# Kernel tuning notes

Hardware: AMD Instinct MI355X
Metric: run time of the kernel (lower is better)

The kernel has to match this reference:

```python
import jax, jax.numpy as jnp
from jax import lax
import numpy as np

B, P, ENC, DEC, ATT, E, S, V = 32, 196, 512, 512, 512, 256, 128, 10000

def setup_inputs() -> dict:
    key = jax.random.key(0)
    ks = jax.random.split(key, 20)
    g = lambda k, shape, s=0.02: jax.random.normal(k, shape, dtype=jnp.float32) * s
    return {
        'features': jax.random.normal(ks[0], (B, P, ENC), dtype=jnp.float32),
        'captions': jax.random.randint(ks[1], (B, S), 0, V, dtype=jnp.int64),
        'emb': g(ks[2], (V, E)),
        'W_enc_att': g(ks[3], (ENC, ATT)), 'b_enc_att': jnp.zeros((ATT,), jnp.float32),
        'W_dec_att': g(ks[4], (DEC, ATT)), 'b_dec_att': jnp.zeros((ATT,), jnp.float32),
        'v_att': g(ks[5], (ATT,)), 'b_full_att': jnp.zeros((), jnp.float32),
        'W_init_h': g(ks[6], (ENC, DEC)), 'b_init_h': jnp.zeros((DEC,), jnp.float32),
        'W_init_c': g(ks[7], (ENC, DEC)), 'b_init_c': jnp.zeros((DEC,), jnp.float32),
        'W_ih': g(ks[8], (4 * DEC, E + ENC)), 'W_hh': g(ks[9], (4 * DEC, DEC)),
        'b_ih': jnp.zeros((4 * DEC,), jnp.float32), 'b_hh': jnp.zeros((4 * DEC,), jnp.float32),
        'W_fcn': g(ks[10], (DEC, V)), 'b_fcn': jnp.zeros((V,), jnp.float32),
    }

def reference(features, captions, emb, W_enc_att, b_enc_att, W_dec_att, b_dec_att,
              v_att, b_full_att, W_init_h, b_init_h, W_init_c, b_init_c,
              W_ih, W_hh, b_ih, b_hh, W_fcn, b_fcn):
    # init hidden state from mean encoder features
    mean_f = features.mean(axis=1)                    # [B, ENC]
    h = mean_f @ W_init_h + b_init_h                  # [B, DEC]
    c = mean_f @ W_init_c + b_init_c
    embeds = emb[captions]                            # [B, S, E]
    feat_proj = features @ W_enc_att + b_enc_att      # [B, P, ATT], loop-invariant

    def step(carry, emb_t):
        h, c = carry
        # additive attention: tanh(Uf + Wh) . v -> softmax -> weighted sum
        att = jnp.tanh(feat_proj + (h @ W_dec_att + b_dec_att)[:, None, :])  # [B, P, ATT]
        scores = att @ v_att + b_full_att             # [B, P]
        alpha = jax.nn.softmax(scores, axis=1)
        context = jnp.einsum('bp,bpe->be', alpha, features)  # [B, ENC]
        x = jnp.concatenate([emb_t, context], axis=1)  # [B, E+ENC]
        gates = x @ W_ih.T + b_ih + h @ W_hh.T + b_hh  # [B, 4*DEC]
        i, f, g, o = jnp.split(gates, 4, axis=1)
        c_new = jax.nn.sigmoid(f) * c + jax.nn.sigmoid(i) * jnp.tanh(g)
        h_new = jax.nn.sigmoid(o) * jnp.tanh(c_new)
        out = h_new @ W_fcn + b_fcn                    # dropout = identity (eval)
        return (h_new, c_new), out

    xs = jnp.swapaxes(embeds[:, :S - 1], 0, 1)         # [S-1, B, E]
    _, preds = lax.scan(step, (h, c), xs)              # [S-1, B, V]
    return jnp.swapaxes(preds, 0, 1)                   # [B, S-1, V]
```

## Files before the change

kernel.cpp:

```cpp
#include <hip/hip_runtime.h>
#include <hip/hip_bf16.h>
#include <stdint.h>

#define BB 32
#define PP 196
#define ENC 512
#define DEC 512
#define ATTD 512
#define EE 256
#define SS 128
#define VV 10000
#define TT 127
#define NBLK 512

typedef unsigned short ushort_t;
typedef unsigned int uint_t;
typedef unsigned long long u64_t;
typedef float f32x4 __attribute__((ext_vector_type(4)));
typedef short s16x8 __attribute__((ext_vector_type(8)));

__device__ __forceinline__ float bf2f(ushort_t u) {
    uint_t x = ((uint_t)u) << 16;
    return __uint_as_float(x);
}
__device__ __forceinline__ float bflo(uint_t u) { return __uint_as_float(u << 16); }
__device__ __forceinline__ float bfhi(uint_t u) { return __uint_as_float(u & 0xffff0000u); }
__device__ __forceinline__ ushort_t f2bf(float f) {
    uint_t u = __float_as_uint(f);
    uint_t r = (u + 0x7FFFu + ((u >> 16) & 1u)) >> 16;
    return (ushort_t)r;
}
__device__ __forceinline__ float ftanh(float x) {
    x = fminf(15.f, fmaxf(-15.f, x));
    float e = __expf(2.f * x);
    return (e - 1.f) / (e + 1.f);
}
__device__ __forceinline__ float fsig(float x) {
    return 1.f / (1.f + __expf(-x));
}

__device__ __forceinline__ float aload1(const float* p) {
    return __hip_atomic_load(p, __ATOMIC_RELAXED, __HIP_MEMORY_SCOPE_AGENT);
}
__device__ __forceinline__ void astore1(float* p, float v) {
    __hip_atomic_store(p, v, __ATOMIC_RELAXED, __HIP_MEMORY_SCOPE_AGENT);
}
__device__ __forceinline__ float2 aload2(const float* p) {
    u64_t v = __hip_atomic_load((const u64_t*)p, __ATOMIC_RELAXED, __HIP_MEMORY_SCOPE_AGENT);
    float2 r;
    r.x = __uint_as_float((uint_t)v);
    r.y = __uint_as_float((uint_t)(v >> 32));
    return r;
}


__global__ void k_cvt(const float* __restrict__ s, ushort_t* __restrict__ d, int n) {
    for (int i = blockIdx.x * blockDim.x + threadIdx.x; i < n; i += gridDim.x * blockDim.x)
        d[i] = f2bf(s[i]);
}

__global__ void k_cvtD(const float* __restrict__ Wdec, ushort_t* __restrict__ out) {
    const int n = DEC * ATTD;
    for (int i = blockIdx.x * blockDim.x + threadIdx.x; i < n; i += gridDim.x * blockDim.x) {
        int k = i & (ATTD - 1);
        int j = i >> 9;
        out[i] = f2bf(Wdec[(size_t)k * ATTD + j]);
    }
}

__global__ void k_embed_bf(const int* __restrict__ cap, const float* __restrict__ emb,
                           ushort_t* __restrict__ out) {
    const int n = TT * BB * EE;
    for (int i = blockIdx.x * blockDim.x + threadIdx.x; i < n; i += gridDim.x * blockDim.x) {
        int e = i & (EE - 1);
        int b = (i >> 8) & (BB - 1);
        int t = i >> 13;
        int tok = cap[b * SS + t];
        out[i] = f2bf(emb[(size_t)tok * EE + e]);
    }
}

__global__ void k_cvtT(const float* __restrict__ Wih, ushort_t* __restrict__ out) {
    const int n = EE * 4 * DEC;
    for (int i = blockIdx.x * blockDim.x + threadIdx.x; i < n; i += gridDim.x * blockDim.x) {
        int k = i & (EE - 1);
        int row = i >> 8;
        out[(size_t)k * (4 * DEC) + row] = f2bf(Wih[(size_t)row * (EE + ENC) + k]);
    }
}

__global__ void k_cvtG2(const float* __restrict__ Wih, const float* __restrict__ Whh,
                        ushort_t* __restrict__ out) {
    const int n = 16 * 2 * 64 * 128 * 8;
    for (int i = blockIdx.x * blockDim.x + threadIdx.x; i < n; i += gridDim.x * blockDim.x) {
        int j = i & 7;
        int R = (i >> 3) & 127;
        int kc = (i >> 10) & 63;
        int kh = (i >> 16) & 1;
        int pcg = i >> 17;
        int d = pcg * 32 + (R >> 2);
        int gate = R & 3;
        int row = gate * DEC + d;
        int k = kh * 512 + kc * 8 + j;
        float v = (k < 512) ? Wih[(size_t)row * (EE + ENC) + EE + k]
                            : Whh[(size_t)row * DEC + (k - 512)];
        out[i] = f2bf(v);
    }
}

__global__ void k_bsum(const float* __restrict__ a, const float* __restrict__ b,
                       float* __restrict__ o, int n) {
    int i = blockIdx.x * blockDim.x + threadIdx.x;
    if (i < n) o[i] = a[i] + b[i];
}

__global__ __launch_bounds__(256) void k_init(const float* __restrict__ feat,
                                              const float* __restrict__ Wh, const float* __restrict__ bh,
                                              const float* __restrict__ Wc, const float* __restrict__ bc,
                                              float* __restrict__ h0, float* __restrict__ c0,
                                              int* __restrict__ bar) {
    __shared__ float ms[ENC];
    int b = blockIdx.x, t = threadIdx.x;
    if (b == 0) {
        for (int i = t; i < 4096; i += 256) bar[i] = 0;
    }
    for (int c = t; c < ENC; c += 256) {
        float s = 0.f;
        for (int p = 0; p < PP; ++p) s += feat[((size_t)b * PP + p) * ENC + c];
        ms[c] = s * (1.f / (float)PP);
    }
    __syncthreads();
    int d0 = 2 * t;
    float ah0 = 0.f, ah1 = 0.f, ac0 = 0.f, ac1 = 0.f;
    for (int k = 0; k < ENC; ++k) {
        float mk = ms[k];
        float2 wh = *(const float2*)(Wh + (size_t)k * DEC + d0);
        float2 wc = *(const float2*)(Wc + (size_t)k * DEC + d0);
        ah0 += mk * wh.x; ah1 += mk * wh.y;
        ac0 += mk * wc.x; ac1 += mk * wc.y;
    }
    h0[b * DEC + d0] = ah0 + bh[d0];
    h0[b * DEC + d0 + 1] = ah1 + bh[d0 + 1];
    c0[b * DEC + d0] = ac0 + bc[d0];
    c0[b * DEC + d0 + 1] = ac1 + bc[d0 + 1];
}

template <int MODE>
__global__ __launch_bounds__(256) void k_gemm(const ushort_t* __restrict__ A,
                                              const ushort_t* __restrict__ Bm,
                                              const float* __restrict__ bias,
                                              ushort_t* __restrict__ outb,
                                              float* __restrict__ outf,
                                              int M, int N, int K) {
    __shared__ __align__(16) ushort_t As[128 * 32];
    __shared__ __align__(16) ushort_t Bs[128 * 32];

    const int tid = threadIdx.x;
    const int wid = tid >> 6, lane = tid & 63;
    const int wm = wid >> 1, wn = wid & 1;
    const int lr = lane & 15, lk = (lane >> 4) * 8;
    const int row0 = blockIdx.x * 128, col0 = blockIdx.y * 128;

    f32x4 acc[4][4];
#pragma unroll
    for (int i = 0; i < 4; ++i)
#pragma unroll
        for (int j = 0; j < 4; ++j) acc[i][j] = (f32x4){0.f, 0.f, 0.f, 0.f};

    for (int k0 = 0; k0 < K; k0 += 32) {
        {
            int r = tid >> 1, kk = (tid & 1) * 16;
            int gr = row0 + r;
            uint4 v0 = {0, 0, 0, 0}, v1 = {0, 0, 0, 0};
            if (gr < M) {
                const ushort_t* sp = A + (size_t)gr * K + k0 + kk;
                v0 = *(const uint4*)sp;
                v1 = *(const uint4*)(sp + 8);
            }
            *(uint4*)(As + r * 32 + kk) = v0;
            *(uint4*)(As + r * 32 + kk + 8) = v1;
        }
        {
            int kk = tid >> 3;
            int n = (tid & 7) * 16;
            const ushort_t* sp = Bm + (size_t)(k0 + kk) * N + col0 + n;
            ushort_t tmp[16];
            if (col0 + n + 16 <= N) {
                *(uint4*)tmp = *(const uint4*)sp;
                *(uint4*)(tmp + 8) = *(const uint4*)(sp + 8);
            } else {
#pragma unroll
                for (int j = 0; j < 16; ++j) {
                    int c = col0 + n + j;
                    tmp[j] = (c < N) ? sp[j] : (ushort_t)0;
                }
            }
#pragma unroll
            for (int j = 0; j < 16; ++j) Bs[(n + j) * 32 + kk] = tmp[j];
        }
        __syncthreads();
        s16x8 af[4], bfr[4];
#pragma unroll
        for (int i = 0; i < 4; ++i)
            af[i] = *(const s16x8*)(As + (wm * 64 + i * 16 + lr) * 32 + lk);
#pragma unroll
        for (int j = 0; j < 4; ++j)
            bfr[j] = *(const s16x8*)(Bs + (wn * 64 + j * 16 + lr) * 32 + lk);
#pragma unroll
        for (int i = 0; i < 4; ++i)
#pragma unroll
            for (int j = 0; j < 4; ++j)
                acc[i][j] = __builtin_amdgcn_mfma_f32_16x16x32_bf16(af[i], bfr[j], acc[i][j], 0, 0, 0);
        __syncthreads();
    }

    const int lrow = (lane >> 4) * 4;
#pragma unroll
    for (int i = 0; i < 4; ++i) {
#pragma unroll
        for (int j = 0; j < 4; ++j) {
            int gr0 = row0 + wm * 64 + i * 16 + lrow;
            int gc = col0 + wn * 64 + j * 16 + lr;
#pragma unroll
            for (int r = 0; r < 4; ++r) {
                int gr = gr0 + r;
                if (gr < M && gc < N) {
                    float v = acc[i][j][r] + bias[gc];
                    if (MODE == 0) {
                        outb[(size_t)gr * N + gc] = f2bf(v);
                    } else {
                        int t = gr >> 5, b = gr & 31;
                        outf[((size_t)(b * TT + t)) * VV + gc] = v;
                    }
                }
            }
        }
    }
}


__device__ __forceinline__ void gbar16(int* cnt, int target) {
    asm volatile("s_waitcnt vmcnt(0)" ::: "memory");
    __syncthreads();
    if (threadIdx.x == 0) {
        __hip_atomic_fetch_add(cnt, 1, __ATOMIC_RELAXED, __HIP_MEMORY_SCOPE_AGENT);
        while (__hip_atomic_load(cnt, __ATOMIC_RELAXED, __HIP_MEMORY_SCOPE_AGENT) < target)
            __builtin_amdgcn_s_sleep(1);
    }
    __syncthreads();
}

__global__ __launch_bounds__(256) void k_steps(
    const ushort_t* __restrict__ fp, const ushort_t* __restrict__ fb,
    const ushort_t* __restrict__ WdecT, const float* __restrict__ bdec,
    const float* __restrict__ vatt, const float* __restrict__ bfull,
    const ushort_t* __restrict__ Wg2, const ushort_t* __restrict__ gemb,
    float* __restrict__ hbuf, const float* __restrict__ cbuf,
    float* __restrict__ a_glob, float* __restrict__ ctxP, float* __restrict__ Sp,
    ushort_t* __restrict__ Hb, int* __restrict__ bar) {

    __shared__ __align__(16) float hs[8 * 68];
    __shared__ __align__(16) float as_[512];
    __shared__ __align__(16) float vs[512];
    __shared__ __align__(16) float cs[512];
    __shared__ __align__(16) float pctx[4 * 520];
    __shared__ float ep[16];
    __shared__ float sS[1];

    const int bid = blockIdx.x, tid = threadIdx.x;
    const float bfull_r = bfull[0];

    const int q = bid & 7, r = bid >> 3;
    const int pcg = 2 * q + (r & 1);
    const int bA = r >> 1;
    int* grpcnt = bar + 576 + bA * 32;

    const int aj = tid >> 3, akh = tid & 7;
    const int j_abs = pcg * 32 + aj;
    const float bdec_r = bdec[j_abs];
    const int pl = tid >> 4, ks = tid & 15;
    const int cnt_b = (pcg < 4) ? 13 : 12;
    const int p0 = (pcg < 4) ? pcg * 13 : 52 + (pcg - 4) * 12;
    const int ps = tid >> 6, cg = tid & 63;
    const int R = tid >> 1, ckh = tid & 1;
    const int cd = pcg * 32 + (R >> 2);
    const int cgate = R & 3;
    const int crow = cgate * DEC + cd;
    const ushort_t* wgp = Wg2 + ((size_t)(pcg * 2 + ckh) * 64) * 1024 + R * 8;

    float creg = ((tid & 7) == 0) ? cbuf[bA * DEC + cd] : 0.f;

    vs[tid] = vatt[tid];
    vs[tid + 256] = vatt[tid + 256];
    __syncthreads();

    for (int st = 0; st < TT; ++st) {
        const float* h_in = hbuf + (size_t)(st & 1) * BB * DEC;
        float* h_out = hbuf + (size_t)((st + 1) & 1) * BB * DEC;

        {
            float2 hv = aload2(h_in + bA * DEC + 2 * tid);
            int k0 = 2 * tid, k1 = 2 * tid + 1;
            hs[(k0 >> 6) * 68 + (k0 & 63)] = hv.x;
            hs[(k1 >> 6) * 68 + (k1 & 63)] = hv.y;
        }
        __syncthreads();
        {
            const ushort_t* wp = WdecT + (size_t)j_abs * 512 + akh * 64;
            const float* hp = hs + akh * 68;
            float acc = 0.f;
#pragma unroll
            for (int c = 0; c < 8; ++c) {
                uint4 wv = *(const uint4*)(wp + c * 8);
                f32x4 x0 = *(const f32x4*)(hp + c * 8);
                f32x4 x1 = *(const f32x4*)(hp + c * 8 + 4);
                acc += bflo(wv.x) * x0[0] + bfhi(wv.x) * x0[1]
                     + bflo(wv.y) * x0[2] + bfhi(wv.y) * x0[3]
                     + bflo(wv.z) * x1[0] + bfhi(wv.z) * x1[1]
                     + bflo(wv.w) * x1[2] + bfhi(wv.w) * x1[3];
            }
            acc += __shfl_xor(acc, 1);
            acc += __shfl_xor(acc, 2);
            acc += __shfl_xor(acc, 4);
            if (akh == 0) astore1(a_glob + bA * ATTD + j_abs, acc + bdec_r);
        }
        gbar16(grpcnt, 16 * (3 * st + 1));

        {
            float2 av = aload2(a_glob + bA * ATTD + 2 * tid);
            as_[2 * tid] = av.x;
            as_[2 * tid + 1] = av.y;
        }
        __syncthreads();
        {
            float acc = 0.f;
            if (pl < cnt_b) {
                const int p = p0 + pl;
                const ushort_t* fr = fp + ((size_t)bA * PP + p) * ATTD + ks * 32;
#pragma unroll
                for (int c2 = 0; c2 < 4; ++c2) {
                    uint4 fv = *(const uint4*)(fr + c2 * 8);
                    const int k = ks * 32 + c2 * 8;
                    const float* ap = as_ + k;
                    const float* vp = vs + k;
                    acc += ftanh(bflo(fv.x) + ap[0]) * vp[0];
                    acc += ftanh(bfhi(fv.x) + ap[1]) * vp[1];
                    acc += ftanh(bflo(fv.y) + ap[2]) * vp[2];
                    acc += ftanh(bfhi(fv.y) + ap[3]) * vp[3];
                    acc += ftanh(bflo(fv.z) + ap[4]) * vp[4];
                    acc += ftanh(bfhi(fv.z) + ap[5]) * vp[5];
                    acc += ftanh(bflo(fv.w) + ap[6]) * vp[6];
                    acc += ftanh(bfhi(fv.w) + ap[7]) * vp[7];
                }
            }
            acc += __shfl_xor(acc, 1);
            acc += __shfl_xor(acc, 2);
            acc += __shfl_xor(acc, 4);
            acc += __shfl_xor(acc, 8);
            if (ks == 0) ep[pl] = (pl < cnt_b) ? __expf(acc + bfull_r) : 0.f;
        }
        __syncthreads();
        if (tid < 16) {
            float v = ep[tid];
            v += __shfl_xor(v, 1);
            v += __shfl_xor(v, 2);
            v += __shfl_xor(v, 4);
            v += __shfl_xor(v, 8);
            if (tid == 0) astore1(Sp + bA * 16 + pcg, v);
        }
        {
            float a8[8];
#pragma unroll
            for (int i2 = 0; i2 < 8; ++i2) a8[i2] = 0.f;
            for (int p2 = ps; p2 < cnt_b; p2 += 4) {
                float e2 = ep[p2];
                uint4 fv = *(const uint4*)(fb + ((size_t)bA * PP + p0 + p2) * ENC + cg * 8);
                a8[0] += e2 * bflo(fv.x); a8[1] += e2 * bfhi(fv.x);
                a8[2] += e2 * bflo(fv.y); a8[3] += e2 * bfhi(fv.y);
                a8[4] += e2 * bflo(fv.z); a8[5] += e2 * bfhi(fv.z);
                a8[6] += e2 * bflo(fv.w); a8[7] += e2 * bfhi(fv.w);
            }
            float* pp = pctx + ps * 520 + cg * 8;
            *(f32x4*)pp = (f32x4){a8[0], a8[1], a8[2], a8[3]};
            *(f32x4*)(pp + 4) = (f32x4){a8[4], a8[5], a8[6], a8[7]};
        }
        __syncthreads();
        {
            int c0i = 2 * tid, c1i = 2 * tid + 1;
            float s0 = pctx[c0i] + pctx[520 + c0i] + pctx[1040 + c0i] + pctx[1560 + c0i];
            float s1 = pctx[c1i] + pctx[520 + c1i] + pctx[1040 + c1i] + pctx[1560 + c1i];
            float* cp = ctxP + ((size_t)bA * 16 + pcg) * 512;
            astore1(cp + c0i, s0);
            astore1(cp + c1i, s1);
        }
        gbar16(grpcnt, 16 * (3 * st + 2));

        {
            if (tid < 16) {
                float s = aload1(Sp + bA * 16 + tid);
                s += __shfl_xor(s, 1);
                s += __shfl_xor(s, 2);
                s += __shfl_xor(s, 4);
                s += __shfl_xor(s, 8);
                if (tid == 0) sS[0] = s;
            }
            __syncthreads();
            const float invS = 1.f / sS[0];
            float s0 = 0.f, s1 = 0.f;
            const float* cp = ctxP + (size_t)bA * 16 * 512 + 2 * tid;
#pragma unroll
            for (int sl = 0; sl < 16; ++sl) {
                float2 v = aload2(cp + sl * 512);
                s0 += v.x;
                s1 += v.y;
            }
            cs[2 * tid] = s0 * invS;
            cs[2 * tid + 1] = s1 * invS;
        }
        __syncthreads();
        {
            float acc = 0.f;
#pragma unroll 8
            for (int kc = 0; kc < 64; ++kc) {
                uint4 wv = *(const uint4*)(wgp + kc * 1024);
                const float* xp = ckh ? (hs + (kc >> 3) * 68 + (kc & 7) * 8) : (cs + kc * 8);
                f32x4 x0 = *(const f32x4*)xp;
                f32x4 x1 = *(const f32x4*)(xp + 4);
                acc += bflo(wv.x) * x0[0] + bfhi(wv.x) * x0[1]
                     + bflo(wv.y) * x0[2] + bfhi(wv.y) * x0[3]
                     + bflo(wv.z) * x1[0] + bfhi(wv.z) * x1[1]
                     + bflo(wv.w) * x1[2] + bfhi(wv.w) * x1[3];
            }
            acc += __shfl_xor(acc, 1);
            const size_t trow = (size_t)st * BB + bA;
            acc += bf2f(gemb[trow * (4 * DEC) + crow]);
            float pf = __shfl_xor(acc, 2);
            float pg = __shfl_xor(acc, 4);
            float po = __shfl_xor(acc, 6);
            if ((tid & 7) == 0) {
                float cn = fsig(pf) * creg + fsig(acc) * ftanh(pg);
                float hn = fsig(po) * ftanh(cn);
                creg = cn;
                astore1(h_out + bA * DEC + cd, hn);
                Hb[trow * DEC + cd] = f2bf(hn);
            }
        }
        gbar16(grpcnt, 16 * (3 * st + 3));
    }
}


extern "C" void kernel_launch(void* const* d_in, const int* in_sizes, int n_in,
                              void* d_out, int out_size, void* d_ws, size_t ws_size,
                              hipStream_t stream) {
    const float* features  = (const float*)d_in[0];
    const int*   captions  = (const int*)d_in[1];
    const float* emb       = (const float*)d_in[2];
    const float* W_enc_att = (const float*)d_in[3];
    const float* b_enc_att = (const float*)d_in[4];
    const float* W_dec_att = (const float*)d_in[5];
    const float* b_dec_att = (const float*)d_in[6];
    const float* v_att     = (const float*)d_in[7];
    const float* b_full    = (const float*)d_in[8];
    const float* W_init_h  = (const float*)d_in[9];
    const float* b_init_h  = (const float*)d_in[10];
    const float* W_init_c  = (const float*)d_in[11];
    const float* b_init_c  = (const float*)d_in[12];
    const float* W_ih      = (const float*)d_in[13];
    const float* W_hh      = (const float*)d_in[14];
    const float* b_ih      = (const float*)d_in[15];
    const float* b_hh      = (const float*)d_in[16];
    const float* W_fcn     = (const float*)d_in[17];
    const float* b_fcn     = (const float*)d_in[18];
    float* out = (float*)d_out;
    char* ws = (char*)d_ws;

    size_t o = 0;
    ushort_t* Wfcn_b  = (ushort_t*)(ws + o); o += (size_t)DEC * VV * 2;
    ushort_t* Wenc_b  = (ushort_t*)(ws + o); o += (size_t)ENC * ATTD * 2;
    ushort_t* WdecT   = (ushort_t*)(ws + o); o += (size_t)DEC * ATTD * 2;
    ushort_t* fb      = (ushort_t*)(ws + o); o += (size_t)BB * PP * ENC * 2;
    ushort_t* fp_b    = (ushort_t*)(ws + o); o += (size_t)BB * PP * ATTD * 2;
    ushort_t* emb_bf  = (ushort_t*)(ws + o); o += (size_t)TT * BB * EE * 2;
    ushort_t* WihT    = (ushort_t*)(ws + o); o += (size_t)EE * 4 * DEC * 2;
    ushort_t* gembuf  = (ushort_t*)(ws + o); o += (size_t)TT * BB * 4 * DEC * 2;
    ushort_t* Wg2     = (ushort_t*)(ws + o); o += (size_t)4 * DEC * 1024 * 2;
    float*    bsum    = (float*)(ws + o);    o += (size_t)4 * DEC * 4;
    ushort_t* Hb      = (ushort_t*)(ws + o); o += (size_t)TT * BB * DEC * 2;
    float*    hbuf    = (float*)(ws + o);    o += (size_t)2 * BB * DEC * 4;
    float*    cbuf    = (float*)(ws + o);    o += (size_t)BB * DEC * 4;
    float*    a_glob  = (float*)(ws + o);    o += (size_t)BB * ATTD * 4;
    float*    ctxP    = (float*)(ws + o);    o += (size_t)BB * 16 * 512 * 4;
    float*    Sp      = (float*)(ws + o);    o += (size_t)BB * 16 * 4 + 64;
    int*      bar     = (int*)(ws + o);      o += 4096 * 4;

    k_cvt<<<2048, 256, 0, stream>>>(W_fcn, Wfcn_b, DEC * VV);
    k_cvt<<<256, 256, 0, stream>>>(W_enc_att, Wenc_b, ENC * ATTD);
    k_cvtD<<<256, 256, 0, stream>>>(W_dec_att, WdecT);
    k_cvt<<<2048, 256, 0, stream>>>(features, fb, BB * PP * ENC);
    k_embed_bf<<<1024, 256, 0, stream>>>(captions, emb, emb_bf);
    k_cvtT<<<1024, 256, 0, stream>>>(W_ih, WihT);
    k_cvtG2<<<4096, 256, 0, stream>>>(W_ih, W_hh, Wg2);
    k_bsum<<<8, 256, 0, stream>>>(b_ih, b_hh, bsum, 4 * DEC);
    k_init<<<32, 256, 0, stream>>>(features, W_init_h, b_init_h, W_init_c, b_init_c,
                                   hbuf, cbuf, bar);
    k_gemm<0><<<dim3((BB * PP) / 128, ATTD / 128), 256, 0, stream>>>(
        fb, Wenc_b, b_enc_att, fp_b, nullptr, BB * PP, ATTD, ENC);
    k_gemm<0><<<dim3((TT * BB + 127) / 128, (4 * DEC) / 128), 256, 0, stream>>>(
        emb_bf, WihT, bsum, gembuf, nullptr, TT * BB, 4 * DEC, EE);

    k_steps<<<NBLK, 256, 0, stream>>>(fp_b, fb, WdecT, b_dec_att, v_att, b_full,
                                      Wg2, gembuf, hbuf, cbuf,
                                      a_glob, ctxP, Sp, Hb, bar);

    k_gemm<1><<<dim3((TT * BB + 127) / 128, (VV + 127) / 128), 256, 0, stream>>>(
        Hb, Wfcn_b, b_fcn, nullptr, out, TT * BB, VV, DEC);
}
```

Baseline: 2.786 ms.

## Split grid barrier into arrive/wait and prefetch operands across barriers

Splits the group barrier into separate arrive and wait phases so that global loads of the feature-projection rows, feature rows, the first gate-weight chunks and the gate embedding are issued while waiting. The W_dec_att slice and the first eight gate-weight vectors are kept in registers across all steps instead of being reloaded every step. It also pads the LDS layout of the attention and v vectors to avoid bank conflicts, splits the gate accumulator in two to shorten the dependency chain, and sets a launch bound of two blocks per SM. The main risk is higher register pressure from the many held uint4 vectors, which could cause spills under the two-block bound.

```diff
diff --git a/kernel.cpp b/kernel.cpp
--- a/kernel.cpp
+++ b/kernel.cpp
@@ -239,18 +239,21 @@
 }
 
 
-__device__ __forceinline__ void gbar16(int* cnt, int target) {
+__device__ __forceinline__ void gbar_arrive(int* cnt) {
     asm volatile("s_waitcnt vmcnt(0)" ::: "memory");
     __syncthreads();
+    if (threadIdx.x == 0)
+        __hip_atomic_fetch_add(cnt, 1, __ATOMIC_RELAXED, __HIP_MEMORY_SCOPE_AGENT);
+}
+__device__ __forceinline__ void gbar_wait(int* cnt, int target) {
     if (threadIdx.x == 0) {
-        __hip_atomic_fetch_add(cnt, 1, __ATOMIC_RELAXED, __HIP_MEMORY_SCOPE_AGENT);
         while (__hip_atomic_load(cnt, __ATOMIC_RELAXED, __HIP_MEMORY_SCOPE_AGENT) < target)
             __builtin_amdgcn_s_sleep(1);
     }
     __syncthreads();
 }
 
-__global__ __launch_bounds__(256) void k_steps(
+__global__ __launch_bounds__(256, 2) void k_steps(
     const ushort_t* __restrict__ fp, const ushort_t* __restrict__ fb,
     const ushort_t* __restrict__ WdecT, const float* __restrict__ bdec,
     const float* __restrict__ vatt, const float* __restrict__ bfull,
@@ -260,8 +263,8 @@
     ushort_t* __restrict__ Hb, int* __restrict__ bar) {
 
     __shared__ __align__(16) float hs[8 * 68];
-    __shared__ __align__(16) float as_[512];
-    __shared__ __align__(16) float vs[512];
+    __shared__ __align__(16) float asS[544];
+    __shared__ __align__(16) float vsS[544];
     __shared__ __align__(16) float cs[512];
     __shared__ __align__(16) float pctx[4 * 520];
     __shared__ float ep[16];
@@ -284,34 +287,47 @@
     const int ps = tid >> 6, cg = tid & 63;
     const int R = tid >> 1, ckh = tid & 1;
     const int cd = pcg * 32 + (R >> 2);
-    const int cgate = R & 3;
-    const int crow = cgate * DEC + cd;
+    const int crow = (R & 3) * DEC + cd;
     const ushort_t* wgp = Wg2 + ((size_t)(pcg * 2 + ckh) * 64) * 1024 + R * 8;
 
     float creg = ((tid & 7) == 0) ? cbuf[bA * DEC + cd] : 0.f;
 
-    vs[tid] = vatt[tid];
-    vs[tid + 256] = vatt[tid + 256];
+    uint4 wdv[8];
+    {
+        const ushort_t* wpA = WdecT + (size_t)j_abs * 512 + akh * 64;
+#pragma unroll
+        for (int c = 0; c < 8; ++c) wdv[c] = *(const uint4*)(wpA + c * 8);
+    }
+    uint4 wgv0[8];
+#pragma unroll
+    for (int kc = 0; kc < 8; ++kc) wgv0[kc] = *(const uint4*)(wgp + kc * 1024);
+
+    {
+        int k0 = tid, k1 = tid + 256;
+        vsS[(k0 & 31) + (k0 >> 5) * 34] = vatt[k0];
+        vsS[(k1 & 31) + (k1 >> 5) * 34] = vatt[k1];
+    }
     __syncthreads();
 
     for (int st = 0; st < TT; ++st) {
         const float* h_in = hbuf + (size_t)(st & 1) * BB * DEC;
         float* h_out = hbuf + (size_t)((st + 1) & 1) * BB * DEC;
+        const size_t trow = (size_t)st * BB + bA;
 
         {
             float2 hv = aload2(h_in + bA * DEC + 2 * tid);
-            int k0 = 2 * tid, k1 = 2 * tid + 1;
-            hs[(k0 >> 6) * 68 + (k0 & 63)] = hv.x;
-            hs[(k1 >> 6) * 68 + (k1 & 63)] = hv.y;
-        }
-        __syncthreads();
-        {
-            const ushort_t* wp = WdecT + (size_t)j_abs * 512 + akh * 64;
+            int k0 = 2 * tid;
+            float* hrow = hs + (k0 >> 6) * 68 + (k0 & 63);
+            hrow[0] = hv.x;
+            hrow[1] = hv.y;
+        }
+        __syncthreads();
+        {
             const float* hp = hs + akh * 68;
             float acc = 0.f;
 #pragma unroll
             for (int c = 0; c < 8; ++c) {
-                uint4 wv = *(const uint4*)(wp + c * 8);
+                uint4 wv = wdv[c];
                 f32x4 x0 = *(const f32x4*)(hp + c * 8);
                 f32x4 x1 = *(const f32x4*)(hp + c * 8 + 4);
                 acc += bflo(wv.x) * x0[0] + bfhi(wv.x) * x0[1]
@@ -324,33 +340,51 @@
             acc += __shfl_xor(acc, 4);
             if (akh == 0) astore1(a_glob + bA * ATTD + j_abs, acc + bdec_r);
         }
-        gbar16(grpcnt, 16 * (3 * st + 1));
+        gbar_arrive(grpcnt);
+        uint4 fpv[4], fbv[4];
+        {
+            int p = p0 + ((pl < cnt_b) ? pl : 0);
+            const ushort_t* fr = fp + ((size_t)bA * PP + p) * ATTD + ks * 32;
+#pragma unroll
+            for (int c2 = 0; c2 < 4; ++c2) fpv[c2] = *(const uint4*)(fr + c2 * 8);
+#pragma unroll
+            for (int j2 = 0; j2 < 4; ++j2) {
+                int p2 = ps + 4 * j2;
+                if (p2 > cnt_b - 1) p2 = cnt_b - 1;
+                fbv[j2] = *(const uint4*)(fb + ((size_t)bA * PP + p0 + p2) * ENC + cg * 8);
+            }
+        }
+        gbar_wait(grpcnt, 16 * (3 * st + 1));
 
         {
             float2 av = aload2(a_glob + bA * ATTD + 2 * tid);
-            as_[2 * tid] = av.x;
-            as_[2 * tid + 1] = av.y;
+            int k0 = 2 * tid;
+            float* arow = asS + (k0 & 31) + (k0 >> 5) * 34;
+            arow[0] = av.x;
+            arow[1] = av.y;
         }
         __syncthreads();
         {
             float acc = 0.f;
             if (pl < cnt_b) {
-                const int p = p0 + pl;
-                const ushort_t* fr = fp + ((size_t)bA * PP + p) * ATTD + ks * 32;
+                const float* ap = asS + ks * 34;
+                const float* vp = vsS + ks * 34;
 #pragma unroll
                 for (int c2 = 0; c2 < 4; ++c2) {
-                    uint4 fv = *(const uint4*)(fr + c2 * 8);
-                    const int k = ks * 32 + c2 * 8;
-                    const float* ap = as_ + k;
-                    const float* vp = vs + k;
-                    acc += ftanh(bflo(fv.x) + ap[0]) * vp[0];
-                    acc += ftanh(bfhi(fv.x) + ap[1]) * vp[1];
-                    acc += ftanh(bflo(fv.y) + ap[2]) * vp[2];
-                    acc += ftanh(bfhi(fv.y) + ap[3]) * vp[3];
-                    acc += ftanh(bflo(fv.z) + ap[4]) * vp[4];
-                    acc += ftanh(bfhi(fv.z) + ap[5]) * vp[5];
-                    acc += ftanh(bflo(fv.w) + ap[6]) * vp[6];
-                    acc += ftanh(bfhi(fv.w) + ap[7]) * vp[7];
+                    uint4 fv = fpv[c2];
+                    const int c = c2 * 8;
+                    float2 a0 = *(const float2*)(ap + c),     a1 = *(const float2*)(ap + c + 2);
+                    float2 a2 = *(const float2*)(ap + c + 4), a3 = *(const float2*)(ap + c + 6);
+                    float2 v0 = *(const float2*)(vp + c),     v1 = *(const float2*)(vp + c + 2);
+                    float2 v2 = *(const float2*)(vp + c + 4), v3 = *(const float2*)(vp + c + 6);
+                    acc += ftanh(bflo(fv.x) + a0.x) * v0.x;
+                    acc += ftanh(bfhi(fv.x) + a0.y) * v0.y;
+                    acc += ftanh(bflo(fv.y) + a1.x) * v1.x;
+                    acc += ftanh(bfhi(fv.y) + a1.y) * v1.y;
+                    acc += ftanh(bflo(fv.z) + a2.x) * v2.x;
+                    acc += ftanh(bfhi(fv.z) + a2.y) * v2.y;
+                    acc += ftanh(bflo(fv.w) + a3.x) * v3.x;
+                    acc += ftanh(bfhi(fv.w) + a3.y) * v3.y;
                 }
             }
             acc += __shfl_xor(acc, 1);
@@ -372,13 +406,17 @@
             float a8[8];
 #pragma unroll
             for (int i2 = 0; i2 < 8; ++i2) a8[i2] = 0.f;
-            for (int p2 = ps; p2 < cnt_b; p2 += 4) {
-                float e2 = ep[p2];
-                uint4 fv = *(const uint4*)(fb + ((size_t)bA * PP + p0 + p2) * ENC + cg * 8);
-                a8[0] += e2 * bflo(fv.x); a8[1] += e2 * bfhi(fv.x);
-                a8[2] += e2 * bflo(fv.y); a8[3] += e2 * bfhi(fv.y);
-                a8[4] += e2 * bflo(fv.z); a8[5] += e2 * bfhi(fv.z);
-                a8[6] += e2 * bflo(fv.w); a8[7] += e2 * bfhi(fv.w);
+#pragma unroll
+            for (int j2 = 0; j2 < 4; ++j2) {
+                int p2 = ps + 4 * j2;
+                if (p2 < cnt_b) {
+                    float e2 = ep[p2];
+                    uint4 fv = fbv[j2];
+                    a8[0] += e2 * bflo(fv.x); a8[1] += e2 * bfhi(fv.x);
+                    a8[2] += e2 * bflo(fv.y); a8[3] += e2 * bfhi(fv.y);
+                    a8[4] += e2 * bflo(fv.z); a8[5] += e2 * bfhi(fv.z);
+                    a8[6] += e2 * bflo(fv.w); a8[7] += e2 * bfhi(fv.w);
+                }
             }
             float* pp = pctx + ps * 520 + cg * 8;
             *(f32x4*)pp = (f32x4){a8[0], a8[1], a8[2], a8[3]};
@@ -393,9 +431,22 @@
             astore1(cp + c0i, s0);
             astore1(cp + c1i, s1);
         }
-        gbar16(grpcnt, 16 * (3 * st + 2));
-
-        {
+        gbar_arrive(grpcnt);
+        uint4 wgv1[8];
+#pragma unroll
+        for (int kc2 = 0; kc2 < 8; ++kc2) wgv1[kc2] = *(const uint4*)(wgp + (8 + kc2) * 1024);
+        const float gembv = bf2f(gemb[trow * (4 * DEC) + crow]);
+        gbar_wait(grpcnt, 16 * (3 * st + 2));
+
+        {
+            float s0 = 0.f, s1 = 0.f;
+            const float* cp = ctxP + (size_t)bA * 16 * 512 + 2 * tid;
+#pragma unroll
+            for (int sl = 0; sl < 16; ++sl) {
+                float2 v = aload2(cp + sl * 512);
+                s0 += v.x;
+                s1 += v.y;
+            }
             if (tid < 16) {
                 float s = aload1(Sp + bA * 16 + tid);
                 s += __shfl_xor(s, 1);
@@ -406,34 +457,49 @@
             }
             __syncthreads();
             const float invS = 1.f / sS[0];
-            float s0 = 0.f, s1 = 0.f;
-            const float* cp = ctxP + (size_t)bA * 16 * 512 + 2 * tid;
-#pragma unroll
-            for (int sl = 0; sl < 16; ++sl) {
-                float2 v = aload2(cp + sl * 512);
-                s0 += v.x;
-                s1 += v.y;
-            }
             cs[2 * tid] = s0 * invS;
             cs[2 * tid + 1] = s1 * invS;
         }
         __syncthreads();
         {
-            float acc = 0.f;
+            float acc0 = 0.f, acc1 = 0.f;
+#pragma unroll
+            for (int kc = 0; kc < 8; ++kc) {
+                uint4 wv = wgv0[kc];
+                const float* xp = ckh ? (hs + (kc >> 3) * 68 + (kc & 7) * 8) : (cs + kc * 8);
+                f32x4 x0 = *(const f32x4*)xp;
+                f32x4 x1 = *(const f32x4*)(xp + 4);
+                acc0 += bflo(wv.x) * x0[0] + bfhi(wv.x) * x0[1]
+                      + bflo(wv.y) * x0[2] + bfhi(wv.y) * x0[3];
+                acc1 += bflo(wv.z) * x1[0] + bfhi(wv.z) * x1[1]
+                      + bflo(wv.w) * x1[2] + bfhi(wv.w) * x1[3];
+            }
+#pragma unroll
+            for (int kc2 = 0; kc2 < 8; ++kc2) {
+                int kc = 8 + kc2;
+                uint4 wv = wgv1[kc2];
+                const float* xp = ckh ? (hs + (kc >> 3) * 68 + (kc & 7) * 8) : (cs + kc * 8);
+                f32x4 x0 = *(const f32x4*)xp;
+                f32x4 x1 = *(const f32x4*)(xp + 4);
+                acc0 += bflo(wv.x) * x0[0] + bfhi(wv.x) * x0[1]
+                      + bflo(wv.y) * x0[2] + bfhi(wv.y) * x0[3];
+                acc1 += bflo(wv.z) * x1[0] + bfhi(wv.z) * x1[1]
+                      + bflo(wv.w) * x1[2] + bfhi(wv.w) * x1[3];
+            }
 #pragma unroll 8
-            for (int kc = 0; kc < 64; ++kc) {
+            for (int kc = 16; kc < 64; ++kc) {
                 uint4 wv = *(const uint4*)(wgp + kc * 1024);
                 const float* xp = ckh ? (hs + (kc >> 3) * 68 + (kc & 7) * 8) : (cs + kc * 8);
                 f32x4 x0 = *(const f32x4*)xp;
                 f32x4 x1 = *(const f32x4*)(xp + 4);
-                acc += bflo(wv.x) * x0[0] + bfhi(wv.x) * x0[1]
-                     + bflo(wv.y) * x0[2] + bfhi(wv.y) * x0[3]
-                     + bflo(wv.z) * x1[0] + bfhi(wv.z) * x1[1]
-                     + bflo(wv.w) * x1[2] + bfhi(wv.w) * x1[3];
-            }
+                acc0 += bflo(wv.x) * x0[0] + bfhi(wv.x) * x0[1]
+                      + bflo(wv.y) * x0[2] + bfhi(wv.y) * x0[3];
+                acc1 += bflo(wv.z) * x1[0] + bfhi(wv.z) * x1[1]
+                      + bflo(wv.w) * x1[2] + bfhi(wv.w) * x1[3];
+            }
+            float acc = acc0 + acc1;
             acc += __shfl_xor(acc, 1);
-            const size_t trow = (size_t)st * BB + bA;
-            acc += bf2f(gemb[trow * (4 * DEC) + crow]);
+            acc += gembv;
             float pf = __shfl_xor(acc, 2);
             float pg = __shfl_xor(acc, 4);
             float po = __shfl_xor(acc, 6);
@@ -445,7 +511,8 @@
                 Hb[trow * DEC + cd] = f2bf(hn);
             }
         }
-        gbar16(grpcnt, 16 * (3 * st + 3));
+        gbar_arrive(grpcnt);
+        gbar_wait(grpcnt, 16 * (3 * st + 3));
     }
 }
 
```

New measurement: 4.759 ms. 1.71x slower.
